# Performance work log

Hardware: AMD Instinct MI355X
Metric: run time of the kernel (lower is better)

## Reference

```python
import jax, jax.numpy as jnp
import numpy as np

B, N, D, L = 4, 16384, 1024, 4
NEG = -10000.0


def setup_inputs() -> dict:
    key = jax.random.key(0)
    k1, k2, k3, k4, k5 = jax.random.split(key, 5)
    xs = jax.random.normal(k1, (B, N, D), dtype=jnp.float32)
    valid = jax.random.randint(k2, (B, N), 0, 2).astype(jnp.bool_)
    # ensure at least one valid instance per bag
    valid = valid.at[:, 0].set(True)
    w1 = jax.random.normal(k3, (D, 1), dtype=jnp.float32) * (1.0 / np.sqrt(D))
    w2 = jax.random.normal(k4, (D, 1), dtype=jnp.float32) * (1.0 / np.sqrt(D))
    wf = jax.random.normal(k5, (L, D), dtype=jnp.float32) * (1.0 / np.sqrt(D))
    return {"xs": xs, "valid": valid, "w1": w1, "w2": w2, "wf": wf}


def reference(xs, valid, w1, w2, wf):
    # gated attention scores: tanh(x w1) * sigmoid(x w2)  -> [B, N]
    a = jnp.tanh(xs @ w1)[..., 0] * jax.nn.sigmoid(xs @ w2)[..., 0]
    # padding mask fill (matches a[~valid] = -10000)
    a = jnp.where(valid, a, NEG)
    att = jax.nn.softmax(a, axis=-1)            # [B, N]
    z = jnp.einsum('bn,bnd->bd', att, xs)       # weighted-sum pooling
    return z @ wf.T                              # [B, L]
```

## Files before the change

kernel.cpp:

```cpp
#include <hip/hip_runtime.h>
#include <hip/hip_bf16.h>
#include <math.h>


#define NB   4
#define NN   16384
#define DD   1024
#define LL   4
#define RPB  16
#define RPW  4
#define GX   (NN / RPB)
#define NBLK (GX * NB)

struct POut { float pd[LL]; float s; float pad[3]; };

__device__ __forceinline__ float wave_reduce(float v) {
    #pragma unroll
    for (int off = 32; off > 0; off >>= 1) v += __shfl_xor(v, off, 64);
    return v;
}

__device__ __forceinline__ float fast_rcp(float x) {
    return __builtin_amdgcn_rcpf(x);
}

__device__ __forceinline__ int popnext(unsigned& m) {
    if (m == 0u) return -1;
    const int i = (int)__builtin_ctz(m);
    m &= m - 1u;
    return i;
}

__global__ __launch_bounds__(256) void abmil_main(
    const float* __restrict__ xs, const void* __restrict__ valid,
    const float* __restrict__ w1, const float* __restrict__ w2,
    const float* __restrict__ wf, POut* __restrict__ parts) {
    const int blk  = blockIdx.x;
    const int bag  = blockIdx.y;
    const int tid  = threadIdx.x;
    const int wave = tid >> 6;
    const int lane = tid & 63;

    const unsigned wd = ((const unsigned*)valid)[lane & 15];
    const unsigned long long bi = __ballot(wd != 0u && wd != 1u);
    const unsigned long long bf = __ballot(wd != 0u && wd != 0x3F800000u);
    const int mode = (bi == 0ull) ? 1 : ((bf == 0ull) ? 2 : 0);

    const float4* w1v = (const float4*)w1;
    const float4* w2v = (const float4*)w2;
    float4 w1r[4], w2r[4];
    #pragma unroll
    for (int k = 0; k < 4; ++k) {
        w1r[k] = w1v[k * 64 + lane];
        w2r[k] = w2v[k * 64 + lane];
    }

    const int n0 = blk * RPB + wave * RPW;
    int flag = 0;
    if (lane < RPW) {
        const size_t idx = (size_t)bag * NN + n0 + lane;
        if (mode == 1)      flag = ((const int*)valid)[idx] != 0;
        else if (mode == 2) flag = ((const float*)valid)[idx] != 0.0f;
        else                flag = ((const unsigned char*)valid)[idx] != 0;
    }
    unsigned m = (unsigned)(__ballot(flag) & ((1u << RPW) - 1u));

    float s = 0.0f;
    float4 z[4];
    #pragma unroll
    for (int k = 0; k < 4; ++k) z[k] = make_float4(0.f, 0.f, 0.f, 0.f);

    const float4* xbase = (const float4*)(xs + (size_t)bag * NN * DD);

    auto loadrow = [&](float4 (&xr)[4], int idx) {
        if (idx >= 0) {
            const float4* xp = xbase + (size_t)(n0 + idx) * (DD / 4);
            #pragma unroll
            for (int k = 0; k < 4; ++k) xr[k] = xp[k * 64 + lane];
        }
    };
    auto comprow = [&](const float4 (&xr)[4]) {
        float d1 = 0.f, d2 = 0.f;
        #pragma unroll
        for (int k = 0; k < 4; ++k) {
            d1 += xr[k].x * w1r[k].x + xr[k].y * w1r[k].y +
                  xr[k].z * w1r[k].z + xr[k].w * w1r[k].w;
            d2 += xr[k].x * w2r[k].x + xr[k].y * w2r[k].y +
                  xr[k].z * w2r[k].z + xr[k].w * w2r[k].w;
        }
        #pragma unroll
        for (int off = 32; off > 0; off >>= 1) {
            d1 += __shfl_xor(d1, off, 64);
            d2 += __shfl_xor(d2, off, 64);
        }
        const float e  = __expf(-2.0f * fabsf(d1));
        const float tn = copysignf((1.0f - e) * fast_rcp(1.0f + e), d1);
        const float sg = fast_rcp(1.0f + __expf(-d2));
        const float p  = __expf(tn * sg);
        s += p;
        #pragma unroll
        for (int k = 0; k < 4; ++k) {
            z[k].x += p * xr[k].x; z[k].y += p * xr[k].y;
            z[k].z += p * xr[k].z; z[k].w += p * xr[k].w;
        }
    };

    float4 xA[4], xB[4];
    int iA = popnext(m), iB = popnext(m);
    loadrow(xA, iA); loadrow(xB, iB);
    while (iA >= 0) {
        comprow(xA); iA = popnext(m); loadrow(xA, iA);
        if (iB < 0) break;
        comprow(xB); iB = popnext(m); loadrow(xB, iB);
    }

    const float4* wfv = (const float4*)wf;
    float pl[LL] = {0.f, 0.f, 0.f, 0.f};
    #pragma unroll
    for (int l = 0; l < LL; ++l) {
        #pragma unroll
        for (int k = 0; k < 4; ++k) {
            const float4 wv = wfv[l * 256 + k * 64 + lane];
            pl[l] += z[k].x * wv.x + z[k].y * wv.y +
                     z[k].z * wv.z + z[k].w * wv.w;
        }
    }
    #pragma unroll
    for (int l = 0; l < LL; ++l) pl[l] = wave_reduce(pl[l]);

    __shared__ float comb[4][LL];
    __shared__ float scomb[4];
    if (lane == 0) {
        #pragma unroll
        for (int l = 0; l < LL; ++l) comb[wave][l] = pl[l];
        scomb[wave] = s;
    }
    __syncthreads();

    POut* po = &parts[(size_t)bag * GX + blk];
    if (tid < LL)
        po->pd[tid] = comb[0][tid] + comb[1][tid] + comb[2][tid] + comb[3][tid];
    if (tid == LL)
        po->s = scomb[0] + scomb[1] + scomb[2] + scomb[3];
}

__global__ __launch_bounds__(256) void abmil_finish(
    const POut* __restrict__ parts, float* __restrict__ out) {
    const int bag  = blockIdx.x;
    const int tid  = threadIdx.x;
    const int wave = tid >> 6;
    const int lane = tid & 63;

    float pd0 = 0.f, pd1 = 0.f, pd2 = 0.f, pd3 = 0.f, s = 0.f;
    #pragma unroll
    for (int j = 0; j < GX / 256; ++j) {
        const POut* p = &parts[(size_t)bag * GX + j * 256 + tid];
        pd0 += p->pd[0]; pd1 += p->pd[1];
        pd2 += p->pd[2]; pd3 += p->pd[3];
        s   += p->s;
    }
    pd0 = wave_reduce(pd0); pd1 = wave_reduce(pd1);
    pd2 = wave_reduce(pd2); pd3 = wave_reduce(pd3);
    s   = wave_reduce(s);

    __shared__ float comb[4][LL + 1];
    if (lane == 0) {
        comb[wave][0] = pd0; comb[wave][1] = pd1;
        comb[wave][2] = pd2; comb[wave][3] = pd3;
        comb[wave][4] = s;
    }
    __syncthreads();
    if (tid == 0) {
        const float st = comb[0][4] + comb[1][4] + comb[2][4] + comb[3][4];
        const float r  = 1.0f / st;
        #pragma unroll
        for (int l = 0; l < LL; ++l)
            out[bag * LL + l] =
                (comb[0][l] + comb[1][l] + comb[2][l] + comb[3][l]) * r;
    }
}

extern "C" void kernel_launch(void* const* d_in, const int* in_sizes, int n_in,
                              void* d_out, int out_size, void* d_ws, size_t ws_size,
                              hipStream_t stream) {
    const float* xs    = (const float*)d_in[0];
    const void*  valid = d_in[1];
    const float* w1    = (const float*)d_in[2];
    const float* w2    = (const float*)d_in[3];
    const float* wf    = (const float*)d_in[4];
    float* out = (float*)d_out;

    POut* parts = (POut*)d_ws;

    dim3 g0(GX, NB);
    abmil_main<<<g0, 256, 0, stream>>>(xs, valid, w1, w2, wf, parts);
    abmil_finish<<<NB, 256, 0, stream>>>(parts, out);
}
```

Measured before the change: 34.44 us.

## Double rows per block and store partials in structure-of-arrays layout

Raises rows per block from 16 to 32 and rows per wave from 4 to 8, halving the grid size and the number of partial results. Partials are now written as separate component arrays rather than padded structs, so the finish kernel reads them with coalesced loads. The aim is less per-block overhead and less finish-kernel traffic, at the cost of fewer blocks for latency hiding.

```diff
diff --git a/kernel.cpp b/kernel.cpp
--- a/kernel.cpp
+++ b/kernel.cpp
@@ -7,12 +7,12 @@
 #define NN   16384
 #define DD   1024
 #define LL   4
-#define RPB  16
-#define RPW  4
+#define RPB  32
+#define RPW  8
 #define GX   (NN / RPB)
 #define NBLK (GX * NB)
 
-struct POut { float pd[LL]; float s; float pad[3]; };
+#define PCOMP 5
 
 __device__ __forceinline__ float wave_reduce(float v) {
     #pragma unroll
@@ -34,7 +34,7 @@
 __global__ __launch_bounds__(256) void abmil_main(
     const float* __restrict__ xs, const void* __restrict__ valid,
     const float* __restrict__ w1, const float* __restrict__ w2,
-    const float* __restrict__ wf, POut* __restrict__ parts) {
+    const float* __restrict__ wf, float* __restrict__ parts) {
     const int blk  = blockIdx.x;
     const int bag  = blockIdx.y;
     const int tid  = threadIdx.x;
@@ -137,37 +137,36 @@
     }
     __syncthreads();
 
-    POut* po = &parts[(size_t)bag * GX + blk];
+    const size_t pidx = (size_t)bag * GX + blk;
     if (tid < LL)
-        po->pd[tid] = comb[0][tid] + comb[1][tid] + comb[2][tid] + comb[3][tid];
+        parts[(size_t)tid * NBLK + pidx] =
+            comb[0][tid] + comb[1][tid] + comb[2][tid] + comb[3][tid];
     if (tid == LL)
-        po->s = scomb[0] + scomb[1] + scomb[2] + scomb[3];
+        parts[(size_t)LL * NBLK + pidx] =
+            scomb[0] + scomb[1] + scomb[2] + scomb[3];
 }
 
 __global__ __launch_bounds__(256) void abmil_finish(
-    const POut* __restrict__ parts, float* __restrict__ out) {
+    const float* __restrict__ parts, float* __restrict__ out) {
     const int bag  = blockIdx.x;
     const int tid  = threadIdx.x;
     const int wave = tid >> 6;
     const int lane = tid & 63;
 
-    float pd0 = 0.f, pd1 = 0.f, pd2 = 0.f, pd3 = 0.f, s = 0.f;
+    float c[PCOMP];
     #pragma unroll
-    for (int j = 0; j < GX / 256; ++j) {
-        const POut* p = &parts[(size_t)bag * GX + j * 256 + tid];
-        pd0 += p->pd[0]; pd1 += p->pd[1];
-        pd2 += p->pd[2]; pd3 += p->pd[3];
-        s   += p->s;
+    for (int q = 0; q < PCOMP; ++q) {
+        float acc = 0.f;
+        #pragma unroll
+        for (int j = 0; j < GX / 256; ++j)
+            acc += parts[(size_t)q * NBLK + (size_t)bag * GX + j * 256 + tid];
+        c[q] = wave_reduce(acc);
     }
-    pd0 = wave_reduce(pd0); pd1 = wave_reduce(pd1);
-    pd2 = wave_reduce(pd2); pd3 = wave_reduce(pd3);
-    s   = wave_reduce(s);
 
-    __shared__ float comb[4][LL + 1];
+    __shared__ float comb[4][PCOMP];
     if (lane == 0) {
-        comb[wave][0] = pd0; comb[wave][1] = pd1;
-        comb[wave][2] = pd2; comb[wave][3] = pd3;
-        comb[wave][4] = s;
+        #pragma unroll
+        for (int q = 0; q < PCOMP; ++q) comb[wave][q] = c[q];
     }
     __syncthreads();
     if (tid == 0) {
@@ -190,7 +189,7 @@
     const float* wf    = (const float*)d_in[4];
     float* out = (float*)d_out;
 
-    POut* parts = (POut*)d_ws;
+    float* parts = (float*)d_ws;
 
     dim3 g0(GX, NB);
     abmil_main<<<g0, 256, 0, stream>>>(xs, valid, w1, w2, wf, parts);
```

New measurement: 31.13 us. 9.6% less time.
